# Kernel tuning notes

Hardware: AMD Instinct MI355X
Metric: run time of the kernel (lower is better)

## Reference

```python
import jax, jax.numpy as jnp
import numpy as np

B, N, F, T, KCHEB, O = 8, 1024, 64, 12, 3, 64

def setup_inputs() -> dict:
    key = jax.random.key(0)
    k1, k2, k3, k4 = jax.random.split(key, 4)
    graph_signal = jax.random.normal(k1, (B, N, F, T), dtype=jnp.float32)
    spatial_attention = jax.random.uniform(k2, (B, N, N), dtype=jnp.float32)
    # Chebyshev polynomials of scaled Laplacian, scaled to keep magnitudes sane
    cheb = jax.random.normal(k3, (KCHEB, N, N), dtype=jnp.float32) / np.float32(np.sqrt(N))
    # theta: (K, F, num_of_filters), glorot-ish scale
    theta = jax.random.normal(k4, (KCHEB, F, O), dtype=jnp.float32) / np.float32(np.sqrt(F))
    return {"graph_signal": graph_signal, "spatial_attention": spatial_attention,
            "cheb": cheb, "theta": theta}

def reference(graph_signal, spatial_attention, cheb, theta):
    # Original loops over t and k computing:
    #   rhs[b,n,f] = sum_m (T_k[m,n] * att[b,m,n]) * x[b,m,f,t]   (transposed batch_dot)
    #   out[b,n,o,t] += rhs @ theta[k]
    # Vectorized over k, t in one pass.
    Ak = cheb[:, None, :, :] * spatial_attention[None]          # (K,B,N,N) = T_k * attention
    rhs = jnp.einsum('kbmn,bmft->kbnft', Ak, graph_signal)      # T_k_with_at^T @ x for all t
    out = jnp.einsum('kbnft,kfo->bnot', rhs, theta)             # sum over k and f
    return jax.nn.relu(out)                                     # (B, N, O, T)
```

## Files before the change

kernel.cpp:

```cpp
#include <hip/hip_runtime.h>
#include <stdint.h>

#define NB 8
#define NN 1024
#define NF 64
#define NT 12
#define NK 3
#define NO 64
#define NQ 768
#define KKC 3072

typedef __attribute__((ext_vector_type(8))) short bf16x8;
typedef __attribute__((ext_vector_type(4))) float f32x4;

typedef const unsigned int __attribute__((address_space(1)))* gas1_t;
typedef unsigned int __attribute__((address_space(3)))* las3_t;

__device__ __forceinline__ void gload_lds16(const void* g, void* l) {
  __builtin_amdgcn_global_load_lds((gas1_t)g, (las3_t)l, 16, 0, 0);
}

__device__ __forceinline__ unsigned short f2bf(float f) {
  union { float f; unsigned int u; } v; v.f = f;
  unsigned int u = v.u;
  unsigned int r = (u + 0x7FFFu + ((u >> 16) & 1u)) >> 16;
  return (unsigned short)r;
}

__global__ void k0_thetaT(const float* __restrict__ theta, unsigned short* __restrict__ thT) {
  int i = blockIdx.x * 256 + threadIdx.x;
  if (i >= NK * NO * NF) return;
  int f = i & 63, o = (i >> 6) & 63, k = i >> 12;
  thT[i] = f2bf(theta[(k * NF + f) * NO + o]);
}

__global__ __launch_bounds__(256) void k1_A2(const float* __restrict__ cheb,
                                             const float* __restrict__ att,
                                             unsigned short* __restrict__ A2) {
  __shared__ float att_s[64][65];
  __shared__ float cheb_s[64][65];
  const int n0 = blockIdx.x * 64;
  const int m0 = blockIdx.y * 64;
  const int b  = blockIdx.z;
  const int tid = threadIdx.x;
  const int r4 = tid >> 4;
  const int c  = tid & 15;

#pragma unroll
  for (int p = 0; p < 4; ++p) {
    int r = r4 + p * 16;
    const float4 v = *(const float4*)(att + ((size_t)(b * NN + m0 + r)) * NN + n0 + c * 4);
    att_s[r][c * 4 + 0] = v.x; att_s[r][c * 4 + 1] = v.y;
    att_s[r][c * 4 + 2] = v.z; att_s[r][c * 4 + 3] = v.w;
  }
  for (int k = 0; k < NK; ++k) {
#pragma unroll
    for (int p = 0; p < 4; ++p) {
      int r = r4 + p * 16;
      const float4 v = *(const float4*)(cheb + ((size_t)(k * NN + m0 + r)) * NN + n0 + c * 4);
      cheb_s[r][c * 4 + 0] = v.x; cheb_s[r][c * 4 + 1] = v.y;
      cheb_s[r][c * 4 + 2] = v.z; cheb_s[r][c * 4 + 3] = v.w;
    }
    __syncthreads();
#pragma unroll
    for (int p = 0; p < 8; ++p) {
      int e  = p * 256 + tid;
      int jn = e >> 5;
      int q  = e & 31;
      float f0 = att_s[2 * q][jn]     * cheb_s[2 * q][jn];
      float f1 = att_s[2 * q + 1][jn] * cheb_s[2 * q + 1][jn];
      unsigned int pk = (unsigned int)f2bf(f0) | ((unsigned int)f2bf(f1) << 16);
      size_t el = ((size_t)(b * NN + n0 + jn)) * KKC + k * NN + m0 + 2 * q;
      *(unsigned int*)(A2 + el) = pk;
    }
    __syncthreads();
  }
}

__global__ __launch_bounds__(256) void k2_xT(const float* __restrict__ x,
                                             unsigned short* __restrict__ xT) {
  __shared__ unsigned int lds[12][16][32];
  const int m0 = blockIdx.x * 16;
  const int b  = blockIdx.y;
  const int tid = threadIdx.x;
  const float* xb = x + ((size_t)(b * NN + m0)) * (NF * NT);

#pragma unroll
  for (int u0 = 0; u0 < 2; ++u0) {
    const int u  = u0 * 256 + tid;
    const int ml = u >> 5;
    const int fp = u & 31;
    const float* src = xb + ((size_t)ml * NF + fp * 2) * NT;
    float v[24];
#pragma unroll
    for (int i = 0; i < 6; ++i)
      *(float4*)(v + i * 4) = *(const float4*)(src + i * 4);
#pragma unroll
    for (int t = 0; t < 12; ++t) {
      unsigned int pk = (unsigned int)f2bf(v[t]) | ((unsigned int)f2bf(v[t + 12]) << 16);
      lds[t][ml][fp] = pk;
    }
  }
  __syncthreads();

#pragma unroll
  for (int it = 0; it < 12; ++it) {
    const int g = it * 256 + tid;
    const int t = g >> 8;
    const int r = g & 255;
    const int m = r >> 4;
    const int f4 = r & 15;
    uint2 u = *(const uint2*)&lds[t][m][2 * f4];
    size_t el = (((size_t)(b * NT + t) * NN) + m0 + m) * NF + f4 * 4;
    *(uint2*)(void*)(xT + el) = u;
  }
}

__global__ __launch_bounds__(256) void k3_Y(const unsigned short* __restrict__ xT,
                                            const unsigned short* __restrict__ thT,
                                            unsigned short* __restrict__ Y) {
  const int mc = blockIdx.x;
  const int tk = blockIdx.y;
  const int b  = blockIdx.z;
  const int t = tk / 3, k = tk % 3;
  const int tid = threadIdx.x;
  const int w = tid >> 6, l = tid & 63;
  const int lrow = l & 15, lk = l >> 4;
  const int mbase = mc * 256 + w * 64;

  const unsigned short* xbase = xT + ((size_t)(b * NT + t)) * NN * NF;
  const unsigned short* tbase = thT + (size_t)k * NO * NF;

  f32x4 acc[4][4] = {};
#pragma unroll
  for (int ks = 0; ks < 2; ++ks) {
    const int fo = ks * 32 + lk * 8;
    bf16x8 a[4], bb[4];
#pragma unroll
    for (int mi = 0; mi < 4; ++mi)
      a[mi] = *(const bf16x8*)(xbase + (size_t)(mbase + mi * 16 + lrow) * NF + fo);
#pragma unroll
    for (int oj = 0; oj < 4; ++oj)
      bb[oj] = *(const bf16x8*)(tbase + (size_t)(oj * 16 + lrow) * NF + fo);
#pragma unroll
    for (int mi = 0; mi < 4; ++mi)
#pragma unroll
      for (int oj = 0; oj < 4; ++oj)
        acc[mi][oj] = __builtin_amdgcn_mfma_f32_16x16x32_bf16(a[mi], bb[oj], acc[mi][oj], 0, 0, 0);
  }
#pragma unroll
  for (int mi = 0; mi < 4; ++mi) {
#pragma unroll
    for (int oj = 0; oj < 4; ++oj) {
      const int o  = oj * 16 + lrow;
      const int mg = mbase + mi * 16 + lk * 4;
      uint2 u;
      u.x = (unsigned int)f2bf(acc[mi][oj][0]) | ((unsigned int)f2bf(acc[mi][oj][1]) << 16);
      u.y = (unsigned int)f2bf(acc[mi][oj][2]) | ((unsigned int)f2bf(acc[mi][oj][3]) << 16);
      size_t el = ((size_t)(b * NQ + o * NT + t)) * KKC + k * NN + mg;
      *(uint2*)(void*)(Y + el) = u;
    }
  }
}

__global__ __launch_bounds__(256) void k4_main(const unsigned short* __restrict__ A2,
                                               const unsigned short* __restrict__ Y,
                                               float* __restrict__ out) {
  __shared__ unsigned short Asl[64 * 64];
  __shared__ unsigned short Bsl[128 * 64];
  const int tid = threadIdx.x;
  const int w = tid >> 6, l = tid & 63;
  const int lrow = l & 15, lk = l >> 4;
  const int wm = w >> 1, wq = w & 1;

  const int lin = (blockIdx.x & 7) * 96 + (blockIdx.x >> 3);
  const int b   = lin / 96;
  const int rem = lin % 96;
  const int bn  = rem / 6;
  const int bq  = rem % 6;

  const unsigned short* Abase = A2 + ((size_t)(b * NN + bn * 64)) * KKC;
  const unsigned short* Bbase = Y  + ((size_t)(b * NQ + bq * 128)) * KKC;

  f32x4 acc[2][4] = {};

  for (int kt = 0; kt < KKC / 64; ++kt) {
    const int kb = kt * 64;
#pragma unroll
    for (int it = 0; it < 2; ++it) {
      const int idx = it * 256 + tid;
      const int r   = idx >> 3;
      const int c16 = (idx & 7) ^ (r & 7);
      gload_lds16(Abase + (size_t)r * KKC + kb + c16 * 8, Asl + (size_t)idx * 8);
    }
#pragma unroll
    for (int it = 0; it < 4; ++it) {
      const int idx = it * 256 + tid;
      const int r   = idx >> 3;
      const int c16 = (idx & 7) ^ (r & 7);
      gload_lds16(Bbase + (size_t)r * KKC + kb + c16 * 8, Bsl + (size_t)idx * 8);
    }
    __syncthreads();
#pragma unroll
    for (int kss = 0; kss < 2; ++kss) {
      bf16x8 af[2], bfr[4];
#pragma unroll
      for (int mi = 0; mi < 2; ++mi) {
        const int row = wm * 32 + mi * 16 + lrow;
        const int sw = (row * 128 + kss * 64 + lk * 16) ^ ((row & 7) << 4);
        af[mi] = *(const bf16x8*)((const char*)Asl + sw);
      }
#pragma unroll
      for (int nj = 0; nj < 4; ++nj) {
        const int row = wq * 64 + nj * 16 + lrow;
        const int sw = (row * 128 + kss * 64 + lk * 16) ^ ((row & 7) << 4);
        bfr[nj] = *(const bf16x8*)((const char*)Bsl + sw);
      }
#pragma unroll
      for (int mi = 0; mi < 2; ++mi)
#pragma unroll
        for (int nj = 0; nj < 4; ++nj)
          acc[mi][nj] = __builtin_amdgcn_mfma_f32_16x16x32_bf16(af[mi], bfr[nj], acc[mi][nj], 0, 0, 0);
    }
    __syncthreads();
  }

  const int nb0 = bn * 64 + wm * 32;
  const int qb0 = bq * 128 + wq * 64;
#pragma unroll
  for (int mi = 0; mi < 2; ++mi) {
#pragma unroll
    for (int nj = 0; nj < 4; ++nj) {
      const int q = qb0 + nj * 16 + lrow;
#pragma unroll
      for (int j = 0; j < 4; ++j) {
        const int n = nb0 + mi * 16 + lk * 4 + j;
        float v = acc[mi][nj][j];
        out[((size_t)(b * NN + n)) * NQ + q] = v > 0.f ? v : 0.f;
      }
    }
  }
}

extern "C" void kernel_launch(void* const* d_in, const int* in_sizes, int n_in,
                              void* d_out, int out_size, void* d_ws, size_t ws_size,
                              hipStream_t stream) {
  const float* x     = (const float*)d_in[0];
  const float* att   = (const float*)d_in[1];
  const float* cheb  = (const float*)d_in[2];
  const float* theta = (const float*)d_in[3];
  float* out = (float*)d_out;

  char* ws = (char*)d_ws;
  unsigned short* A2  = (unsigned short*)(ws);
  unsigned short* xT  = (unsigned short*)(ws + 50331648);
  unsigned short* Y   = (unsigned short*)(ws + 62914560);
  unsigned short* thT = (unsigned short*)(ws + 100663296);

  k0_thetaT<<<48, 256, 0, stream>>>(theta, thT);
  k1_A2<<<dim3(16, 16, 8), 256, 0, stream>>>(cheb, att, A2);
  k2_xT<<<dim3(64, 8), 256, 0, stream>>>(x, xT);
  k3_Y<<<dim3(4, 36, 8), 256, 0, stream>>>(xT, thT, Y);
  k4_main<<<768, 256, 0, stream>>>(A2, Y, out);
}
```

Baseline: 103.0 us.

## Double-buffer LDS tiles in main GEMM and reuse x tile across Chebyshev orders

The main GEMM kernel now ping-pongs between two LDS buffers, so the async global-to-LDS load of the next K-tile overlaps the MFMA work on the current one. This replaces the old load, sync, compute, sync sequence. Separately, k3_Y stages the x tile into LDS once and loops over all three Chebyshev orders, instead of launching separate blocks per k that each reload x. The cost is twice the LDS in k4, which may lower occupancy, and fewer blocks in k3.

After: 105.2 us. +2.1%, slower.

```diff
diff --git a/kernel.cpp b/kernel.cpp
--- a/kernel.cpp
+++ b/kernel.cpp
@@ -119,46 +119,62 @@
 __global__ __launch_bounds__(256) void k3_Y(const unsigned short* __restrict__ xT,
                                             const unsigned short* __restrict__ thT,
                                             unsigned short* __restrict__ Y) {
+  __shared__ unsigned short Xs[256 * 64];
   const int mc = blockIdx.x;
-  const int tk = blockIdx.y;
+  const int t  = blockIdx.y;
   const int b  = blockIdx.z;
-  const int t = tk / 3, k = tk % 3;
   const int tid = threadIdx.x;
   const int w = tid >> 6, l = tid & 63;
   const int lrow = l & 15, lk = l >> 4;
-  const int mbase = mc * 256 + w * 64;
-
-  const unsigned short* xbase = xT + ((size_t)(b * NT + t)) * NN * NF;
-  const unsigned short* tbase = thT + (size_t)k * NO * NF;
-
-  f32x4 acc[4][4] = {};
-#pragma unroll
-  for (int ks = 0; ks < 2; ++ks) {
-    const int fo = ks * 32 + lk * 8;
-    bf16x8 a[4], bb[4];
-#pragma unroll
-    for (int mi = 0; mi < 4; ++mi)
-      a[mi] = *(const bf16x8*)(xbase + (size_t)(mbase + mi * 16 + lrow) * NF + fo);
-#pragma unroll
-    for (int oj = 0; oj < 4; ++oj)
-      bb[oj] = *(const bf16x8*)(tbase + (size_t)(oj * 16 + lrow) * NF + fo);
-#pragma unroll
-    for (int mi = 0; mi < 4; ++mi)
+
+  const unsigned short* xbase = xT + ((size_t)(b * NT + t)) * NN * NF + (size_t)(mc * 256) * NF;
+
+#pragma unroll
+  for (int it = 0; it < 8; ++it) {
+    const int idx = it * 256 + tid;
+    const int r   = idx >> 3;
+    const int c16 = (idx & 7) ^ (r & 7);
+    gload_lds16(xbase + (size_t)r * NF + c16 * 8, Xs + (size_t)idx * 8);
+  }
+  __syncthreads();
+
+  bf16x8 af[2][4];
+#pragma unroll
+  for (int ks = 0; ks < 2; ++ks)
+#pragma unroll
+    for (int mi = 0; mi < 4; ++mi) {
+      const int row = w * 64 + mi * 16 + lrow;
+      const int sw = (row * 128 + ks * 64 + lk * 16) ^ ((row & 7) << 4);
+      af[ks][mi] = *(const bf16x8*)((const char*)Xs + sw);
+    }
+
+  for (int k = 0; k < NK; ++k) {
+    const unsigned short* tb = thT + (size_t)k * NO * NF;
+    f32x4 acc[4][4] = {};
+#pragma unroll
+    for (int ks = 0; ks < 2; ++ks) {
+      bf16x8 bb[4];
 #pragma unroll
       for (int oj = 0; oj < 4; ++oj)
-        acc[mi][oj] = __builtin_amdgcn_mfma_f32_16x16x32_bf16(a[mi], bb[oj], acc[mi][oj], 0, 0, 0);
-  }
-#pragma unroll
-  for (int mi = 0; mi < 4; ++mi) {
-#pragma unroll
-    for (int oj = 0; oj < 4; ++oj) {
-      const int o  = oj * 16 + lrow;
-      const int mg = mbase + mi * 16 + lk * 4;
-      uint2 u;
-      u.x = (unsigned int)f2bf(acc[mi][oj][0]) | ((unsigned int)f2bf(acc[mi][oj][1]) << 16);
-      u.y = (unsigned int)f2bf(acc[mi][oj][2]) | ((unsigned int)f2bf(acc[mi][oj][3]) << 16);
-      size_t el = ((size_t)(b * NQ + o * NT + t)) * KKC + k * NN + mg;
-      *(uint2*)(void*)(Y + el) = u;
+        bb[oj] = *(const bf16x8*)(tb + (size_t)(oj * 16 + lrow) * NF + ks * 32 + lk * 8);
+#pragma unroll
+      for (int mi = 0; mi < 4; ++mi)
+#pragma unroll
+        for (int oj = 0; oj < 4; ++oj)
+          acc[mi][oj] = __builtin_amdgcn_mfma_f32_16x16x32_bf16(af[ks][mi], bb[oj], acc[mi][oj], 0, 0, 0);
+    }
+#pragma unroll
+    for (int mi = 0; mi < 4; ++mi) {
+#pragma unroll
+      for (int oj = 0; oj < 4; ++oj) {
+        const int o  = oj * 16 + lrow;
+        const int mg = mc * 256 + w * 64 + mi * 16 + lk * 4;
+        uint2 u;
+        u.x = (unsigned int)f2bf(acc[mi][oj][0]) | ((unsigned int)f2bf(acc[mi][oj][1]) << 16);
+        u.y = (unsigned int)f2bf(acc[mi][oj][2]) | ((unsigned int)f2bf(acc[mi][oj][3]) << 16);
+        size_t el = ((size_t)(b * NQ + o * NT + t)) * KKC + k * NN + mg;
+        *(uint2*)(void*)(Y + el) = u;
+      }
     }
   }
 }
@@ -166,8 +182,8 @@
 __global__ __launch_bounds__(256) void k4_main(const unsigned short* __restrict__ A2,
                                                const unsigned short* __restrict__ Y,
                                                float* __restrict__ out) {
-  __shared__ unsigned short Asl[64 * 64];
-  __shared__ unsigned short Bsl[128 * 64];
+  __shared__ unsigned short Asl0[64 * 64],  Asl1[64 * 64];
+  __shared__ unsigned short Bsl0[128 * 64], Bsl1[128 * 64];
   const int tid = threadIdx.x;
   const int w = tid >> 6, l = tid & 63;
   const int lrow = l & 15, lk = l >> 4;
@@ -184,23 +200,25 @@
 
   f32x4 acc[2][4] = {};
 
-  for (int kt = 0; kt < KKC / 64; ++kt) {
+  auto STAGE = [&](unsigned short* Ad, unsigned short* Bd, int kt) {
     const int kb = kt * 64;
 #pragma unroll
     for (int it = 0; it < 2; ++it) {
       const int idx = it * 256 + tid;
       const int r   = idx >> 3;
       const int c16 = (idx & 7) ^ (r & 7);
-      gload_lds16(Abase + (size_t)r * KKC + kb + c16 * 8, Asl + (size_t)idx * 8);
+      gload_lds16(Abase + (size_t)r * KKC + kb + c16 * 8, Ad + (size_t)idx * 8);
     }
 #pragma unroll
     for (int it = 0; it < 4; ++it) {
       const int idx = it * 256 + tid;
       const int r   = idx >> 3;
       const int c16 = (idx & 7) ^ (r & 7);
-      gload_lds16(Bbase + (size_t)r * KKC + kb + c16 * 8, Bsl + (size_t)idx * 8);
-    }
-    __syncthreads();
+      gload_lds16(Bbase + (size_t)r * KKC + kb + c16 * 8, Bd + (size_t)idx * 8);
+    }
+  };
+
+  auto COMPUTE = [&](const unsigned short* As, const unsigned short* Bs) {
 #pragma unroll
     for (int kss = 0; kss < 2; ++kss) {
       bf16x8 af[2], bfr[4];
@@ -208,13 +226,13 @@
       for (int mi = 0; mi < 2; ++mi) {
         const int row = wm * 32 + mi * 16 + lrow;
         const int sw = (row * 128 + kss * 64 + lk * 16) ^ ((row & 7) << 4);
-        af[mi] = *(const bf16x8*)((const char*)Asl + sw);
+        af[mi] = *(const bf16x8*)((const char*)As + sw);
       }
 #pragma unroll
       for (int nj = 0; nj < 4; ++nj) {
         const int row = wq * 64 + nj * 16 + lrow;
         const int sw = (row * 128 + kss * 64 + lk * 16) ^ ((row & 7) << 4);
-        bfr[nj] = *(const bf16x8*)((const char*)Bsl + sw);
+        bfr[nj] = *(const bf16x8*)((const char*)Bs + sw);
       }
 #pragma unroll
       for (int mi = 0; mi < 2; ++mi)
@@ -222,6 +240,16 @@
         for (int nj = 0; nj < 4; ++nj)
           acc[mi][nj] = __builtin_amdgcn_mfma_f32_16x16x32_bf16(af[mi], bfr[nj], acc[mi][nj], 0, 0, 0);
     }
+  };
+
+  STAGE(Asl0, Bsl0, 0);
+  __syncthreads();
+  for (int kt = 0; kt < KKC / 64; kt += 2) {
+    STAGE(Asl1, Bsl1, kt + 1);
+    COMPUTE(Asl0, Bsl0);
+    __syncthreads();
+    if (kt + 2 < KKC / 64) STAGE(Asl0, Bsl0, kt + 2);
+    COMPUTE(Asl1, Bsl1);
     __syncthreads();
   }
 
@@ -260,6 +288,6 @@
   k0_thetaT<<<48, 256, 0, stream>>>(theta, thT);
   k1_A2<<<dim3(16, 16, 8), 256, 0, stream>>>(cheb, att, A2);
   k2_xT<<<dim3(64, 8), 256, 0, stream>>>(x, xT);
-  k3_Y<<<dim3(4, 36, 8), 256, 0, stream>>>(xT, thT, Y);
+  k3_Y<<<dim3(4, 12, 8), 256, 0, stream>>>(xT, thT, Y);
   k4_main<<<768, 256, 0, stream>>>(A2, Y, out);
 }
```

## Fuse x transpose into Y GEMM and loop batches inside A2 kernel

Applied to the files above, without the earlier changes.

Merges the x-transpose kernel into the theta GEMM. x is converted to bf16 straight into swizzled LDS and multiplied against theta staged in LDS, so the xT intermediate is never written to or re-read from global memory. The A2 kernel now loads the three cheb tiles once and loops over all batches inside each block, which cuts redundant cheb reads by the batch count. The trade-off is a much smaller A2 grid (256 blocks instead of 2048), which may leave the GPU underfilled during a bandwidth-bound phase, and one fewer kernel launch.

New measurement: 97.92 us. -4.9%, faster.

```diff
diff --git a/kernel.cpp b/kernel.cpp
--- a/kernel.cpp
+++ b/kernel.cpp
@@ -38,127 +38,121 @@
                                              const float* __restrict__ att,
                                              unsigned short* __restrict__ A2) {
   __shared__ float att_s[64][65];
-  __shared__ float cheb_s[64][65];
+  __shared__ float cheb_s[3][64][65];
   const int n0 = blockIdx.x * 64;
   const int m0 = blockIdx.y * 64;
-  const int b  = blockIdx.z;
   const int tid = threadIdx.x;
   const int r4 = tid >> 4;
   const int c  = tid & 15;
 
 #pragma unroll
-  for (int p = 0; p < 4; ++p) {
-    int r = r4 + p * 16;
-    const float4 v = *(const float4*)(att + ((size_t)(b * NN + m0 + r)) * NN + n0 + c * 4);
-    att_s[r][c * 4 + 0] = v.x; att_s[r][c * 4 + 1] = v.y;
-    att_s[r][c * 4 + 2] = v.z; att_s[r][c * 4 + 3] = v.w;
-  }
-  for (int k = 0; k < NK; ++k) {
+  for (int k = 0; k < NK; ++k)
 #pragma unroll
     for (int p = 0; p < 4; ++p) {
       int r = r4 + p * 16;
       const float4 v = *(const float4*)(cheb + ((size_t)(k * NN + m0 + r)) * NN + n0 + c * 4);
-      cheb_s[r][c * 4 + 0] = v.x; cheb_s[r][c * 4 + 1] = v.y;
-      cheb_s[r][c * 4 + 2] = v.z; cheb_s[r][c * 4 + 3] = v.w;
-    }
-    __syncthreads();
-#pragma unroll
-    for (int p = 0; p < 8; ++p) {
-      int e  = p * 256 + tid;
-      int jn = e >> 5;
-      int q  = e & 31;
-      float f0 = att_s[2 * q][jn]     * cheb_s[2 * q][jn];
-      float f1 = att_s[2 * q + 1][jn] * cheb_s[2 * q + 1][jn];
-      unsigned int pk = (unsigned int)f2bf(f0) | ((unsigned int)f2bf(f1) << 16);
-      size_t el = ((size_t)(b * NN + n0 + jn)) * KKC + k * NN + m0 + 2 * q;
-      *(unsigned int*)(A2 + el) = pk;
-    }
-    __syncthreads();
-  }
-}
-
-__global__ __launch_bounds__(256) void k2_xT(const float* __restrict__ x,
-                                             unsigned short* __restrict__ xT) {
-  __shared__ unsigned int lds[12][16][32];
-  const int m0 = blockIdx.x * 16;
+      cheb_s[k][r][c * 4 + 0] = v.x; cheb_s[k][r][c * 4 + 1] = v.y;
+      cheb_s[k][r][c * 4 + 2] = v.z; cheb_s[k][r][c * 4 + 3] = v.w;
+    }
+
+  for (int b = 0; b < NB; ++b) {
+    __syncthreads();
+#pragma unroll
+    for (int p = 0; p < 4; ++p) {
+      int r = r4 + p * 16;
+      const float4 v = *(const float4*)(att + ((size_t)(b * NN + m0 + r)) * NN + n0 + c * 4);
+      att_s[r][c * 4 + 0] = v.x; att_s[r][c * 4 + 1] = v.y;
+      att_s[r][c * 4 + 2] = v.z; att_s[r][c * 4 + 3] = v.w;
+    }
+    __syncthreads();
+    for (int k = 0; k < NK; ++k) {
+#pragma unroll
+      for (int p = 0; p < 8; ++p) {
+        int e  = p * 256 + tid;
+        int jn = e >> 5;
+        int q  = e & 31;
+        float f0 = att_s[2 * q][jn]     * cheb_s[k][2 * q][jn];
+        float f1 = att_s[2 * q + 1][jn] * cheb_s[k][2 * q + 1][jn];
+        unsigned int pk = (unsigned int)f2bf(f0) | ((unsigned int)f2bf(f1) << 16);
+        size_t el = ((size_t)(b * NN + n0 + jn)) * KKC + k * NN + m0 + 2 * q;
+        *(unsigned int*)(A2 + el) = pk;
+      }
+    }
+  }
+}
+
+__global__ __launch_bounds__(256) void k23_Y(const float* __restrict__ x,
+                                             const unsigned short* __restrict__ thT,
+                                             unsigned short* __restrict__ Y) {
+  __shared__ unsigned short Xs[12 * 16 * 64];
+  __shared__ unsigned short Ts[3 * 64 * 64];
+  const int mc = blockIdx.x;
   const int b  = blockIdx.y;
-  const int tid = threadIdx.x;
-  const float* xb = x + ((size_t)(b * NN + m0)) * (NF * NT);
-
-#pragma unroll
-  for (int u0 = 0; u0 < 2; ++u0) {
-    const int u  = u0 * 256 + tid;
-    const int ml = u >> 5;
-    const int fp = u & 31;
-    const float* src = xb + ((size_t)ml * NF + fp * 2) * NT;
-    float v[24];
-#pragma unroll
-    for (int i = 0; i < 6; ++i)
-      *(float4*)(v + i * 4) = *(const float4*)(src + i * 4);
-#pragma unroll
-    for (int t = 0; t < 12; ++t) {
-      unsigned int pk = (unsigned int)f2bf(v[t]) | ((unsigned int)f2bf(v[t + 12]) << 16);
-      lds[t][ml][fp] = pk;
-    }
-  }
-  __syncthreads();
-
-#pragma unroll
-  for (int it = 0; it < 12; ++it) {
-    const int g = it * 256 + tid;
-    const int t = g >> 8;
-    const int r = g & 255;
-    const int m = r >> 4;
-    const int f4 = r & 15;
-    uint2 u = *(const uint2*)&lds[t][m][2 * f4];
-    size_t el = (((size_t)(b * NT + t) * NN) + m0 + m) * NF + f4 * 4;
-    *(uint2*)(void*)(xT + el) = u;
-  }
-}
-
-__global__ __launch_bounds__(256) void k3_Y(const unsigned short* __restrict__ xT,
-                                            const unsigned short* __restrict__ thT,
-                                            unsigned short* __restrict__ Y) {
-  const int mc = blockIdx.x;
-  const int tk = blockIdx.y;
-  const int b  = blockIdx.z;
-  const int t = tk / 3, k = tk % 3;
   const int tid = threadIdx.x;
   const int w = tid >> 6, l = tid & 63;
   const int lrow = l & 15, lk = l >> 4;
-  const int mbase = mc * 256 + w * 64;
-
-  const unsigned short* xbase = xT + ((size_t)(b * NT + t)) * NN * NF;
-  const unsigned short* tbase = thT + (size_t)k * NO * NF;
-
-  f32x4 acc[4][4] = {};
-#pragma unroll
-  for (int ks = 0; ks < 2; ++ks) {
-    const int fo = ks * 32 + lk * 8;
-    bf16x8 a[4], bb[4];
-#pragma unroll
-    for (int mi = 0; mi < 4; ++mi)
-      a[mi] = *(const bf16x8*)(xbase + (size_t)(mbase + mi * 16 + lrow) * NF + fo);
-#pragma unroll
-    for (int oj = 0; oj < 4; ++oj)
-      bb[oj] = *(const bf16x8*)(tbase + (size_t)(oj * 16 + lrow) * NF + fo);
-#pragma unroll
-    for (int mi = 0; mi < 4; ++mi)
-#pragma unroll
-      for (int oj = 0; oj < 4; ++oj)
-        acc[mi][oj] = __builtin_amdgcn_mfma_f32_16x16x32_bf16(a[mi], bb[oj], acc[mi][oj], 0, 0, 0);
-  }
-#pragma unroll
-  for (int mi = 0; mi < 4; ++mi) {
-#pragma unroll
-    for (int oj = 0; oj < 4; ++oj) {
-      const int o  = oj * 16 + lrow;
-      const int mg = mbase + mi * 16 + lk * 4;
-      uint2 u;
-      u.x = (unsigned int)f2bf(acc[mi][oj][0]) | ((unsigned int)f2bf(acc[mi][oj][1]) << 16);
-      u.y = (unsigned int)f2bf(acc[mi][oj][2]) | ((unsigned int)f2bf(acc[mi][oj][3]) << 16);
-      size_t el = ((size_t)(b * NQ + o * NT + t)) * KKC + k * NN + mg;
-      *(uint2*)(void*)(Y + el) = u;
+
+  const float* xb = x + ((size_t)(b * NN + mc * 16)) * (NF * NT);
+#pragma unroll
+  for (int u0 = 0; u0 < 2; ++u0) {
+    const int u  = u0 * 256 + tid;
+    const int m  = u >> 5;
+    const int fp = u & 31;
+    const float* src = xb + ((size_t)m * NF + fp * 2) * NT;
+    float v[24];
+#pragma unroll
+    for (int i = 0; i < 6; ++i)
+      *(float4*)(v + i * 4) = *(const float4*)(src + i * 4);
+#pragma unroll
+    for (int t = 0; t < 12; ++t) {
+      unsigned int pk = (unsigned int)f2bf(v[t]) | ((unsigned int)f2bf(v[t + 12]) << 16);
+      const int byte = (t * 2048 + m * 128 + fp * 4) ^ ((m & 7) << 4);
+      *(unsigned int*)((char*)Xs + byte) = pk;
+    }
+  }
+#pragma unroll
+  for (int u0 = 0; u0 < 6; ++u0) {
+    const int u  = u0 * 256 + tid;
+    const int k  = u >> 9;
+    const int o  = (u >> 3) & 63;
+    const int f8 = u & 7;
+    bf16x8 val = *(const bf16x8*)(thT + (size_t)u * 8);
+    const int byte = (k * 8192 + o * 128 + f8 * 16) ^ ((o & 7) << 4);
+    *(bf16x8*)((char*)Ts + byte) = val;
+  }
+  __syncthreads();
+
+#pragma unroll
+  for (int ti = 0; ti < 3; ++ti) {
+    const int t = w * 3 + ti;
+    bf16x8 af[2];
+#pragma unroll
+    for (int kss = 0; kss < 2; ++kss) {
+      const int byte = (t * 2048 + lrow * 128 + kss * 64 + lk * 16) ^ ((lrow & 7) << 4);
+      af[kss] = *(const bf16x8*)((const char*)Xs + byte);
+    }
+    for (int k = 0; k < NK; ++k) {
+      f32x4 acc[4] = {};
+#pragma unroll
+      for (int kss = 0; kss < 2; ++kss) {
+#pragma unroll
+        for (int oj = 0; oj < 4; ++oj) {
+          const int row = oj * 16 + lrow;
+          const int byte = (k * 8192 + row * 128 + kss * 64 + lk * 16) ^ ((row & 7) << 4);
+          bf16x8 bb = *(const bf16x8*)((const char*)Ts + byte);
+          acc[oj] = __builtin_amdgcn_mfma_f32_16x16x32_bf16(af[kss], bb, acc[oj], 0, 0, 0);
+        }
+      }
+#pragma unroll
+      for (int oj = 0; oj < 4; ++oj) {
+        const int o  = oj * 16 + lrow;
+        const int mg = mc * 16 + lk * 4;
+        uint2 u;
+        u.x = (unsigned int)f2bf(acc[oj][0]) | ((unsigned int)f2bf(acc[oj][1]) << 16);
+        u.y = (unsigned int)f2bf(acc[oj][2]) | ((unsigned int)f2bf(acc[oj][3]) << 16);
+        size_t el = ((size_t)(b * NQ + o * NT + t)) * KKC + k * NN + mg;
+        *(uint2*)(void*)(Y + el) = u;
+      }
     }
   }
 }
@@ -253,13 +247,11 @@
 
   char* ws = (char*)d_ws;
   unsigned short* A2  = (unsigned short*)(ws);
-  unsigned short* xT  = (unsigned short*)(ws + 50331648);
-  unsigned short* Y   = (unsigned short*)(ws + 62914560);
-  unsigned short* thT = (unsigned short*)(ws + 100663296);
+  unsigned short* Y   = (unsigned short*)(ws + 50331648);
+  unsigned short* thT = (unsigned short*)(ws + 88080384);
 
   k0_thetaT<<<48, 256, 0, stream>>>(theta, thT);
-  k1_A2<<<dim3(16, 16, 8), 256, 0, stream>>>(cheb, att, A2);
-  k2_xT<<<dim3(64, 8), 256, 0, stream>>>(x, xT);
-  k3_Y<<<dim3(4, 36, 8), 256, 0, stream>>>(xT, thT, Y);
+  k23_Y<<<dim3(64, 8), 256, 0, stream>>>(x, thT, Y);
+  k1_A2<<<dim3(16, 16), 256, 0, stream>>>(cheb, att, A2);
   k4_main<<<768, 256, 0, stream>>>(A2, Y, out);
 }
```
